# Optimization experiments

Measured on AMD Instinct MI355X. Metric: run time of the kernel, lower is better.

## Reference

```python
import jax, jax.numpy as jnp
import numpy as np

A = 15           # anchors per location (5 sizes x 3 ratios)
H, W = 200, 320  # feature map size
N = 8            # batch
STRIDE = 4
PRE_NMS = 2000
POST_NMS = 1000
NMS_THRESH = 0.7
MIN_SIZE = 1.0
SCORE_THRESH = 0.0
BBOX_CLIP = float(np.log(1000.0 / 16.0))  # torchvision BoxCoder clamp on dw/dh


def _make_anchors():
    # torchvision-style cell anchors: ratio-major, then sizes, shifted over the grid.
    sizes = np.array([32.0, 64.0, 128.0, 256.0, 512.0])
    ratios = np.array([0.5, 1.0, 2.0])
    h_r = np.sqrt(ratios)
    w_r = 1.0 / h_r
    ws = (w_r[:, None] * sizes[None, :]).reshape(-1)  # [15]
    hs = (h_r[:, None] * sizes[None, :]).reshape(-1)
    base = np.stack([-ws, -hs, ws, hs], axis=1) / 2.0  # [15,4] centered at 0
    sx = np.arange(W) * STRIDE
    sy = np.arange(H) * STRIDE
    yy, xx = np.meshgrid(sy, sx, indexing="ij")
    shifts = np.stack([xx, yy, xx, yy], axis=-1).reshape(-1, 1, 4)  # [H*W,1,4]
    return (shifts + base[None]).reshape(-1, 4).astype(np.float32)  # [H*W*A,4]


def setup_inputs() -> dict:
    key = jax.random.key(0)
    k1, k2 = jax.random.split(key)
    return {
        "box_cls": jax.random.normal(k1, (N, A, H, W), dtype=jnp.float32),
        "box_regression": jax.random.normal(k2, (N, 4 * A, H, W), dtype=jnp.float32),
        "anchors": jnp.asarray(_make_anchors()),
        "img_h": 800,
        "img_w": 1280,
    }


def _decode(deltas, anchors):
    # BoxCoder.decode with weights (1,1,1,1). deltas [N,K,4], anchors [K,4] xyxy.
    wa = anchors[:, 2] - anchors[:, 0]
    ha = anchors[:, 3] - anchors[:, 1]
    cxa = anchors[:, 0] + 0.5 * wa
    cya = anchors[:, 1] + 0.5 * ha
    dx, dy = deltas[..., 0], deltas[..., 1]
    dw = jnp.minimum(deltas[..., 2], BBOX_CLIP)
    dh = jnp.minimum(deltas[..., 3], BBOX_CLIP)
    cx = dx * wa + cxa
    cy = dy * ha + cya
    w = wa * jnp.exp(dw)
    h = ha * jnp.exp(dh)
    return jnp.stack(
        [cx - 0.5 * w, cy - 0.5 * h, cx + 0.5 * w, cy + 0.5 * h], axis=-1
    )


def _nms_keep(boxes, scores):
    # Greedy NMS over boxes sorted by descending score; scores < 0 mark invalid.
    x1, y1, x2, y2 = boxes[:, 0], boxes[:, 1], boxes[:, 2], boxes[:, 3]
    area = (x2 - x1) * (y2 - y1)
    ix = jnp.maximum(0.0, jnp.minimum(x2[:, None], x2[None, :]) - jnp.maximum(x1[:, None], x1[None, :]))
    iy = jnp.maximum(0.0, jnp.minimum(y2[:, None], y2[None, :]) - jnp.maximum(y1[:, None], y1[None, :]))
    inter = ix * iy
    iou = inter / (area[:, None] + area[None, :] - inter)  # [K,K]
    k = boxes.shape[0]
    idx = jnp.arange(k)
    keep0 = scores >= 0.0

    def body(i, keep):
        sup = keep[i] & (iou[i] > NMS_THRESH) & (idx > i)
        return keep & ~sup

    return jax.lax.fori_loop(0, k, body, keep0)


def reference(box_cls, box_regression, anchors, img_h, img_w):
    n = box_cls.shape[0]
    # permute_and_flatten: [N, A*C, H, W] -> [N, H*W*A, C]
    objectness = box_cls.reshape(n, A, 1, H, W).transpose(0, 3, 4, 1, 2).reshape(n, -1)
    deltas = box_regression.reshape(n, A, 4, H, W).transpose(0, 3, 4, 1, 2).reshape(n, -1, 4)
    proposals = _decode(deltas, anchors)  # [N, K, 4]
    # clip to image (single image size for the whole batch)
    fh = jnp.float32(img_h)
    fw = jnp.float32(img_w)
    proposals = jnp.stack(
        [
            jnp.clip(proposals[..., 0], 0.0, fw),
            jnp.clip(proposals[..., 1], 0.0, fh),
            jnp.clip(proposals[..., 2], 0.0, fw),
            jnp.clip(proposals[..., 3], 0.0, fh),
        ],
        axis=-1,
    )
    # pre-NMS top-k per image (single feature level)
    top_s, top_i = jax.lax.top_k(objectness, PRE_NMS)        # [N, PRE]
    boxes = jnp.take_along_axis(proposals, top_i[..., None], axis=1)  # [N, PRE, 4]
    scores = jax.nn.sigmoid(top_s)
    # remove small boxes and low-scoring boxes (mask instead of dynamic shapes)
    ws = boxes[..., 2] - boxes[..., 0]
    hs = boxes[..., 3] - boxes[..., 1]
    valid = (ws >= MIN_SIZE) & (hs >= MIN_SIZE) & (scores >= SCORE_THRESH)
    scores_m = jnp.where(valid, scores, -1.0)
    order = jnp.argsort(-scores_m, axis=1)
    boxes_s = jnp.take_along_axis(boxes, order[..., None], axis=1)
    scores_s = jnp.take_along_axis(scores_m, order, axis=1)
    keep = jax.vmap(_nms_keep)(boxes_s, scores_s)            # [N, PRE] bool
    ks = jnp.where(keep, scores_s, -1.0)
    fs, fi = jax.lax.top_k(ks, POST_NMS)                     # [N, POST]
    fb = jnp.take_along_axis(boxes_s, fi[..., None], axis=1)
    ok = fs >= 0.0
    final_boxes = jnp.where(ok[..., None], fb, 0.0)          # zero-padded, fixed shape
    final_scores = jnp.where(ok, fs, 0.0)
    return final_boxes, final_scores
```

## Files before the change

### kernel.cpp

```cpp
#include <hip/hip_runtime.h>
#include <hip/hip_bf16.h>
#include <stdint.h>

typedef unsigned long long u64;

#define AN 15
#define HH 200
#define WW 320
#define HWSZ (HH*WW)
#define PER (AN*HWSZ)
#define NB 8
#define K_PRE 2000
#define K_POST 1000
#define SORTN 4096
#define HBINS 4096
#define HBLK 64
#define FSLICE 512
#define NMS_TH 0.7f
#define BBOX_CLIP_F 4.135166556742356f
#define FLOOR12 3072u

#define PHI(x) ((x) + ((x) >> 3))

__device__ __forceinline__ unsigned keyOfU(unsigned u) {
    return (u & 0x80000000u) ? ~u : (u | 0x80000000u);
}
__device__ __forceinline__ float valOf(unsigned k) {
    unsigned u = (k & 0x80000000u) ? (k ^ 0x80000000u) : ~k;
    return __uint_as_float(u);
}

__global__ __launch_bounds__(256)
void k_hc(const uint4* __restrict__ cls4, u64* __restrict__ fbuf,
          unsigned* __restrict__ cnts) {
    int n = blockIdx.y;
    __shared__ unsigned cnt;
    if (threadIdx.x == 0) cnt = 0;
    __syncthreads();
    u64* slice = fbuf + ((size_t)n * HBLK + blockIdx.x) * FSLICE;
    const uint4* p = cls4 + (size_t)n * (PER / 4);
    int stride = gridDim.x * 256;

#define PROC(vv, ii) {                                                        \
        unsigned kk[4] = {keyOfU((vv).x), keyOfU((vv).y), keyOfU((vv).z),     \
                          keyOfU((vv).w)};                                    \
        int i0 = (ii) * 4;                                                    \
        int a = i0 / HWSZ;                                                    \
        int r0 = i0 - a * HWSZ;                                               \
        _Pragma("unroll")                                                     \
        for (int c = 0; c < 4; ++c) {                                         \
            if ((kk[c] >> 20) >= FLOOR12) {                                   \
                unsigned pos = atomicAdd(&cnt, 1u);                           \
                if (pos < FSLICE) {                                           \
                    unsigned idx = (unsigned)((r0 + c) * AN + a);             \
                    slice[pos] = ((u64)kk[c] << 32) | (u64)(~idx);            \
                }                                                             \
            }                                                                 \
        }                                                                     \
    }

    int i = blockIdx.x * 256 + threadIdx.x;
    for (; i + stride < PER / 4; i += 2 * stride) {
        uint4 a4 = p[i];
        uint4 b4 = p[i + stride];
        PROC(a4, i) PROC(b4, i + stride)
    }
    if (i < PER / 4) { uint4 a4 = p[i]; PROC(a4, i) }
#undef PROC

    __syncthreads();
    unsigned c0 = cnt;
    if (threadIdx.x == 0) cnts[n * HBLK + blockIdx.x] = c0;
    unsigned cz = (c0 > FSLICE) ? FSLICE : c0;
    for (unsigned t = cz + threadIdx.x; t < FSLICE; t += 256) slice[t] = 0ull;
}

__global__ __launch_bounds__(512)
void k_mid(const uint4* __restrict__ cls4, const u64* __restrict__ fbuf,
           const unsigned* __restrict__ cnts, const float* __restrict__ reg,
           const float* __restrict__ anchors, const int* __restrict__ pih,
           const int* __restrict__ piw,
           float* __restrict__ boxes_s, float* __restrict__ scores_s) {
    int n = blockIdx.x;
    int tid = threadIdx.x;
    __shared__ unsigned lh[HBINS];
    __shared__ unsigned L[512];
    __shared__ u64 sb[PHI(SORTN - 1) + 1];
    __shared__ unsigned sT12, sMode, fcnt;

    if (tid < HBLK) L[tid] = cnts[n * HBLK + tid];
    __syncthreads();
    if (tid == 0) {
        unsigned tot = 0; unsigned ovf = 0;
        for (int b = 0; b < HBLK; ++b) { tot += L[b]; ovf |= (L[b] > FSLICE); }
        sMode = (tot >= K_PRE && !ovf) ? 0u : 1u;
    }
    __syncthreads();
    unsigned mode = sMode;

    for (int b = tid; b < HBINS; b += 512) lh[b] = 0;
    __syncthreads();
    if (mode == 0) {
        const u64* src = fbuf + (size_t)n * HBLK * FSLICE;
        for (int t = tid; t < HBLK * FSLICE; t += 512) {
            unsigned k12 = (unsigned)(src[t] >> 52);
            if (k12 >= FLOOR12) atomicAdd(&lh[k12], 1u);
        }
    } else {
        const uint4* p = cls4 + (size_t)n * (PER / 4);
        for (int i = tid; i < PER / 4; i += 512) {
            uint4 v = p[i];
            atomicAdd(&lh[keyOfU(v.x) >> 20], 1u);
            atomicAdd(&lh[keyOfU(v.y) >> 20], 1u);
            atomicAdd(&lh[keyOfU(v.z) >> 20], 1u);
            atomicAdd(&lh[keyOfU(v.w) >> 20], 1u);
        }
    }
    __syncthreads();

    unsigned s[8];
    {
        uint4 v0 = *(const uint4*)(lh + 8 * tid);
        uint4 v1 = *(const uint4*)(lh + 8 * tid + 4);
        s[7] = v1.w; s[6] = v1.z + s[7]; s[5] = v1.y + s[6]; s[4] = v1.x + s[5];
        s[3] = v0.w + s[4]; s[2] = v0.z + s[3]; s[1] = v0.y + s[2]; s[0] = v0.x + s[1];
    }
    __syncthreads();
    L[tid] = s[0];
    __syncthreads();
    for (int off = 1; off < 512; off <<= 1) {
        unsigned x = L[tid] + ((tid + off < 512) ? L[tid + off] : 0u);
        __syncthreads(); L[tid] = x; __syncthreads();
    }
    unsigned tail = (tid < 511) ? L[tid + 1] : 0u;
#pragma unroll
    for (int e = 0; e < 8; ++e) {
        unsigned sfE = s[e] + tail;
        unsigned sfN = (e < 7) ? (s[e + 1] + tail) : tail;
        if (sfE >= K_PRE && sfN < K_PRE) sT12 = 8u * tid + e;
    }
    __syncthreads();
    unsigned T12 = sT12;

    if (tid == 0) fcnt = 0;
    __syncthreads();
    if (mode == 0) {
        const u64* src = fbuf + (size_t)n * HBLK * FSLICE;
        for (int t = tid; t < HBLK * FSLICE; t += 512) {
            u64 e = src[t];
            if ((unsigned)(e >> 52) >= T12) {
                unsigned pos = atomicAdd(&fcnt, 1u);
                if (pos < SORTN) sb[PHI((int)pos)] = e;
            }
        }
    } else {
        const uint4* p = cls4 + (size_t)n * (PER / 4);
        for (int i = tid; i < PER / 4; i += 512) {
            uint4 v = p[i];
            unsigned kk[4] = {keyOfU(v.x), keyOfU(v.y), keyOfU(v.z), keyOfU(v.w)};
            int i0 = i * 4;
            int a = i0 / HWSZ;
            int r0 = i0 - a * HWSZ;
#pragma unroll
            for (int c = 0; c < 4; ++c) {
                if ((kk[c] >> 20) >= T12) {
                    unsigned pos = atomicAdd(&fcnt, 1u);
                    if (pos < SORTN) {
                        unsigned idx = (unsigned)((r0 + c) * AN + a);
                        sb[PHI((int)pos)] = ((u64)kk[c] << 32) | (u64)(~idx);
                    }
                }
            }
        }
    }
    __syncthreads();
    unsigned fc = fcnt; if (fc > SORTN) fc = SORTN;
    for (unsigned t = fc + tid; t < SORTN; t += 512) sb[PHI((int)t)] = 0ull;
    __syncthreads();

    u64 r[8];
#define CE(a_, b_, d_) { bool sw_ = (d_) ? (r[a_] < r[b_]) : (r[a_] > r[b_]); \
                         if (sw_) { u64 t_ = r[a_]; r[a_] = r[b_]; r[b_] = t_; } }
    {
#pragma unroll
        for (int e = 0; e < 8; ++e) r[e] = sb[9 * tid + e];
        CE(0, 1, true)  CE(2, 3, false) CE(4, 5, true)  CE(6, 7, false)
        CE(0, 2, true)  CE(1, 3, true)  CE(4, 6, false) CE(5, 7, false)
        CE(0, 1, true)  CE(2, 3, true)  CE(4, 5, false) CE(6, 7, false)
#pragma unroll
        for (int e = 0; e < 8; ++e) sb[9 * tid + e] = r[e];
        __syncthreads();
    }
    for (int k = 8; k <= SORTN; k <<= 1) {
        for (int j = k >> 1; j >= 8; j >>= 1) {
#pragma unroll
            for (int ss = 0; ss < 4; ++ss) {
                int c = tid + ss * 512;
                int i = ((c & ~(j - 1)) << 1) | (c & (j - 1));
                int p = i | j;
                bool dir = (i & k) == 0;
                u64 a = sb[PHI(i)], b = sb[PHI(p)];
                bool sw = dir ? (a < b) : (a > b);
                if (sw) { sb[PHI(i)] = b; sb[PHI(p)] = a; }
            }
            __syncthreads();
        }
        {
            bool d = ((8 * tid) & k) == 0;
#pragma unroll
            for (int e = 0; e < 8; ++e) r[e] = sb[9 * tid + e];
            CE(0, 4, d) CE(1, 5, d) CE(2, 6, d) CE(3, 7, d)
            CE(0, 2, d) CE(1, 3, d) CE(4, 6, d) CE(5, 7, d)
            CE(0, 1, d) CE(2, 3, d) CE(4, 5, d) CE(6, 7, d)
#pragma unroll
            for (int e = 0; e < 8; ++e) sb[9 * tid + e] = r[e];
            __syncthreads();
        }
    }
#undef CE

    float fh = (float)(*pih);
    float fw = (float)(*piw);

    float bx[4][4]; float sc[4]; int pred[4];
#pragma unroll
    for (int q = 0; q < 4; ++q) {
        int t = tid + 512 * q;
        pred[q] = 0; sc[q] = -1.0f;
        bx[q][0] = bx[q][1] = bx[q][2] = bx[q][3] = 0.f;
        if (t < K_PRE) {
            u64 e = sb[PHI(t)];
            unsigned key = (unsigned)(e >> 32);
            unsigned idx = ~((unsigned)e);
            float v = valOf(key);
            float sgm = 1.0f / (1.0f + expf(-v));
            int a = (int)(idx % AN);
            int rr = (int)(idx / AN);
            size_t base = ((size_t)(n * AN + a) * 4) * HWSZ + rr;
            float dx = reg[base];
            float dy = reg[base + HWSZ];
            float dw = reg[base + 2 * (size_t)HWSZ];
            float dh = reg[base + 3 * (size_t)HWSZ];
            float4 an4 = ((const float4*)anchors)[idx];
            float wa = an4.z - an4.x, ha = an4.w - an4.y;
            float cxa = an4.x + 0.5f * wa, cya = an4.y + 0.5f * ha;
            dw = fminf(dw, BBOX_CLIP_F); dh = fminf(dh, BBOX_CLIP_F);
            float cx = dx * wa + cxa, cy = dy * ha + cya;
            float w = wa * expf(dw), h = ha * expf(dh);
            float x1 = cx - 0.5f * w, y1 = cy - 0.5f * h;
            float x2 = cx + 0.5f * w, y2 = cy + 0.5f * h;
            x1 = fminf(fmaxf(x1, 0.f), fw);
            y1 = fminf(fmaxf(y1, 0.f), fh);
            x2 = fminf(fmaxf(x2, 0.f), fw);
            y2 = fminf(fmaxf(y2, 0.f), fh);
            bool valid = ((x2 - x1) >= 1.0f) && ((y2 - y1) >= 1.0f);
            bx[q][0] = x1; bx[q][1] = y1; bx[q][2] = x2; bx[q][3] = y2;
            sc[q] = sgm; pred[q] = valid ? 1 : 0;
        }
    }
    __syncthreads();

    __shared__ u64 ww[32];
    __shared__ int wpfx[33];
    int lane = tid & 63, wid = tid >> 6;
#pragma unroll
    for (int q = 0; q < 4; ++q) {
        u64 bal = __ballot(pred[q] != 0);
        if (lane == 0) ww[wid + 8 * q] = bal;
    }
    __syncthreads();
    if (tid == 0) {
        int acc = 0;
#pragma unroll
        for (int w2 = 0; w2 < 32; ++w2) { wpfx[w2] = acc; acc += (int)__popcll(ww[w2]); }
        wpfx[32] = acc;
    }
    __syncthreads();
    int V = wpfx[32];

#pragma unroll
    for (int q = 0; q < 4; ++q) {
        int t = tid + 512 * q;
        if (t < K_PRE) {
            int wi = t >> 6;
            int before = wpfx[wi] + (int)__popcll(ww[wi] & ((1ull << (unsigned)lane) - 1ull));
            int pos = pred[q] ? before : (V + (t - before));
            float4 b4; b4.x = bx[q][0]; b4.y = bx[q][1]; b4.z = bx[q][2]; b4.w = bx[q][3];
            ((float4*)boxes_s)[(size_t)n * K_PRE + pos] = b4;
            scores_s[(size_t)n * K_PRE + pos] = pred[q] ? sc[q] : -1.0f;
        }
    }
}

__global__ __launch_bounds__(64)
void k_maskT(const float* __restrict__ boxes_s, u64* __restrict__ maskT) {
    int n = blockIdx.y;
    int p = blockIdx.x;
    int lane = threadIdx.x;
    int cb = (int)((sqrtf(8.0f * (float)p + 1.0f) - 1.0f) * 0.5f);
    while ((cb + 1) * (cb + 2) / 2 <= p) ++cb;
    while (cb * (cb + 1) / 2 > p) --cb;
    int rb = p - cb * (cb + 1) / 2;

    __shared__ float rx1[64], ry1[64], rx2[64], ry2[64], rar[64];
    int c = cb * 64 + lane;
    bool cok = c < K_PRE;
    float4 c4; c4.x = c4.y = c4.z = c4.w = 0.f;
    if (cok) c4 = ((const float4*)boxes_s)[(size_t)n * K_PRE + c];
    float areaC = (c4.z - c4.x) * (c4.w - c4.y);

    int r = rb * 64 + lane;
    float4 r4; r4.x = r4.y = r4.z = r4.w = 0.f;
    if (r < K_PRE) r4 = ((const float4*)boxes_s)[(size_t)n * K_PRE + r];
    rx1[lane] = r4.x; ry1[lane] = r4.y; rx2[lane] = r4.z; ry2[lane] = r4.w;
    rar[lane] = (r4.z - r4.x) * (r4.w - r4.y);
    __syncthreads();

    u64 bits = 0;
    int bmax = 0;
    if (cok) { bmax = c - rb * 64; if (bmax > 64) bmax = 64; }
    for (int b = 0; b < bmax; ++b) {
        float ix = fminf(c4.z, rx2[b]) - fmaxf(c4.x, rx1[b]); ix = fmaxf(ix, 0.f);
        float iy = fminf(c4.w, ry2[b]) - fmaxf(c4.y, ry1[b]); iy = fmaxf(iy, 0.f);
        float inter = ix * iy;
        float iou = inter / (rar[b] + areaC - inter);
        if (iou > NMS_TH) bits |= (1ull << b);
    }
    maskT[((size_t)n * 32 + rb) * 2048 + c] = bits;
}

__global__ __launch_bounds__(64)
void k_scanT(const u64* __restrict__ maskT, const float* __restrict__ boxes_s,
             const float* __restrict__ scores_s, float* __restrict__ out) {
    int n = blockIdx.x;
    int lane = threadIdx.x;
    __shared__ float ls[2048];
    __shared__ u64 keptw[32];
    for (int i = lane; i < 500; i += 64)
        ((float4*)ls)[i] = ((const float4*)(scores_s + (size_t)n * K_PRE))[i];
    if (lane < 48) ls[2000 + lane] = -1.0f;
    if (lane < 32) keptw[lane] = 0ull;
    __syncthreads();

    const u64* mb = maskT + (size_t)n * 32 * 2048;
    int kept_total = 0;

    u64 wv[32];
#pragma unroll
    for (int rb = 0; rb < 32; ++rb) wv[rb] = mb[(size_t)rb * 2048 + lane];

    for (int f = 0; f < 32; ++f) {
        int c = f * 64 + lane;

        u64 wn[32];
        if (f < 31) {
            int cn = c + 64;
#pragma unroll
            for (int rb = 0; rb < 32; ++rb) wn[rb] = mb[(size_t)rb * 2048 + cn];
        }

        u64 hit = 0;
#pragma unroll
        for (int rb = 0; rb < 32; ++rb) hit |= (wv[rb] & keptw[rb]);
        bool ext = hit != 0ull;
        u64 diag = wv[f];

        bool v = (ls[c] >= 0.0f) && !ext;
        u64 kept = __ballot(v);
        while (true) {
            u64 nk = __ballot(v && ((diag & kept) == 0ull));
            if (nk == kept) break;
            kept = nk;
        }

        if ((kept >> lane) & 1ull) {
            int rank = kept_total + (int)__popcll(kept & ((1ull << lane) - 1ull));
            if (rank < K_POST) {
                float4 b4 = ((const float4*)boxes_s)[(size_t)n * K_PRE + c];
                ((float4*)out)[(size_t)n * K_POST + rank] = b4;
                out[(size_t)NB * K_POST * 4 + (size_t)n * K_POST + rank] = ls[c];
            }
        }
        kept_total += (int)__popcll(kept);
        if (lane == 0) keptw[f] = kept;
        if (kept_total >= K_POST || f == 31) break;
#pragma unroll
        for (int rb = 0; rb < 32; ++rb) wv[rb] = wn[rb];
    }

    int start = (kept_total < K_POST) ? kept_total : K_POST;
    float4 z4; z4.x = z4.y = z4.z = z4.w = 0.f;
    for (int rk = start + lane; rk < K_POST; rk += 64) {
        ((float4*)out)[(size_t)n * K_POST + rk] = z4;
        out[(size_t)NB * K_POST * 4 + (size_t)n * K_POST + rk] = 0.f;
    }
}

extern "C" void kernel_launch(void* const* d_in, const int* in_sizes, int n_in,
                              void* d_out, int out_size, void* d_ws, size_t ws_size,
                              hipStream_t stream) {
    const float* cls     = (const float*)d_in[0];
    const float* regr    = (const float*)d_in[1];
    const float* anchors = (const float*)d_in[2];
    const int*   pih     = (const int*)d_in[3];
    const int*   piw     = (const int*)d_in[4];
    float* out = (float*)d_out;

    char* w = (char*)d_ws;
    u64*      maskT   = (u64*)(w + 0);
    u64*      fbuf    = (u64*)(w + 4194304);
    unsigned* cnts    = (unsigned*)(w + 6291456);
    float*    boxes_s = (float*)(w + 6293504);
    float*    scores_s= (float*)(w + 6549504);

    k_hc<<<dim3(HBLK, NB), 256, 0, stream>>>((const uint4*)cls, fbuf, cnts);
    k_mid<<<NB, 512, 0, stream>>>((const uint4*)cls, fbuf, cnts, regr, anchors,
                                  pih, piw, boxes_s, scores_s);
    k_maskT<<<dim3(528, NB), 64, 0, stream>>>(boxes_s, maskT);
    k_scanT<<<NB, 64, 0, stream>>>(maskT, boxes_s, scores_s, out);
    (void)in_sizes; (void)n_in; (void)ws_size; (void)out_size;
}
```

Baseline: 144.1 us.

## Split k_mid into separate select, sort and decode kernels

The monolithic per-image k_mid kernel becomes three kernels. k_select builds the histogram and finds the threshold with 1024 threads. k_sort gathers candidates and bitonic-sorts them in shared memory, then writes the top entries to a global candidate buffer. k_decode decodes boxes and compacts valid ones with 1024 threads. The aim is to give each phase a leaner kernel with less shared memory and register pressure and more threads where the work is parallel. In exchange it adds two kernel launches and a global round-trip for the sorted candidates, and still runs only one block per image.

```diff
diff --git a/kernel.cpp b/kernel.cpp
--- a/kernel.cpp
+++ b/kernel.cpp
@@ -75,40 +75,35 @@
     for (unsigned t = cz + threadIdx.x; t < FSLICE; t += 256) slice[t] = 0ull;
 }
 
-__global__ __launch_bounds__(512)
-void k_mid(const uint4* __restrict__ cls4, const u64* __restrict__ fbuf,
-           const unsigned* __restrict__ cnts, const float* __restrict__ reg,
-           const float* __restrict__ anchors, const int* __restrict__ pih,
-           const int* __restrict__ piw,
-           float* __restrict__ boxes_s, float* __restrict__ scores_s) {
-    int n = blockIdx.x;
-    int tid = threadIdx.x;
+__global__ __launch_bounds__(1024)
+void k_select(const uint4* __restrict__ cls4, const u64* __restrict__ fbuf,
+              const unsigned* __restrict__ cnts,
+              unsigned* __restrict__ selT12, unsigned* __restrict__ modeArr) {
+    int n = blockIdx.x, t = threadIdx.x;
     __shared__ unsigned lh[HBINS];
-    __shared__ unsigned L[512];
-    __shared__ u64 sb[PHI(SORTN - 1) + 1];
-    __shared__ unsigned sT12, sMode, fcnt;
-
-    if (tid < HBLK) L[tid] = cnts[n * HBLK + tid];
-    __syncthreads();
-    if (tid == 0) {
-        unsigned tot = 0; unsigned ovf = 0;
+    __shared__ unsigned L[1024];
+    __shared__ unsigned sMode;
+
+    if (t < HBLK) L[t] = cnts[n * HBLK + t];
+    for (int b = t; b < HBINS; b += 1024) lh[b] = 0;
+    __syncthreads();
+    if (t == 0) {
+        unsigned tot = 0, ovf = 0;
         for (int b = 0; b < HBLK; ++b) { tot += L[b]; ovf |= (L[b] > FSLICE); }
         sMode = (tot >= K_PRE && !ovf) ? 0u : 1u;
     }
     __syncthreads();
     unsigned mode = sMode;
 
-    for (int b = tid; b < HBINS; b += 512) lh[b] = 0;
-    __syncthreads();
     if (mode == 0) {
         const u64* src = fbuf + (size_t)n * HBLK * FSLICE;
-        for (int t = tid; t < HBLK * FSLICE; t += 512) {
-            unsigned k12 = (unsigned)(src[t] >> 52);
+        for (int s = t; s < HBLK * FSLICE; s += 1024) {
+            unsigned k12 = (unsigned)(src[s] >> 52);
             if (k12 >= FLOOR12) atomicAdd(&lh[k12], 1u);
         }
     } else {
         const uint4* p = cls4 + (size_t)n * (PER / 4);
-        for (int i = tid; i < PER / 4; i += 512) {
+        for (int i = t; i < PER / 4; i += 1024) {
             uint4 v = p[i];
             atomicAdd(&lh[keyOfU(v.x) >> 20], 1u);
             atomicAdd(&lh[keyOfU(v.y) >> 20], 1u);
@@ -118,38 +113,43 @@
     }
     __syncthreads();
 
-    unsigned s[8];
-    {
-        uint4 v0 = *(const uint4*)(lh + 8 * tid);
-        uint4 v1 = *(const uint4*)(lh + 8 * tid + 4);
-        s[7] = v1.w; s[6] = v1.z + s[7]; s[5] = v1.y + s[6]; s[4] = v1.x + s[5];
-        s[3] = v0.w + s[4]; s[2] = v0.z + s[3]; s[1] = v0.y + s[2]; s[0] = v0.x + s[1];
-    }
-    __syncthreads();
-    L[tid] = s[0];
-    __syncthreads();
-    for (int off = 1; off < 512; off <<= 1) {
-        unsigned x = L[tid] + ((tid + off < 512) ? L[tid + off] : 0u);
-        __syncthreads(); L[tid] = x; __syncthreads();
-    }
-    unsigned tail = (tid < 511) ? L[tid + 1] : 0u;
-#pragma unroll
-    for (int e = 0; e < 8; ++e) {
-        unsigned sfE = s[e] + tail;
-        unsigned sfN = (e < 7) ? (s[e + 1] + tail) : tail;
-        if (sfE >= K_PRE && sfN < K_PRE) sT12 = 8u * tid + e;
-    }
-    __syncthreads();
-    unsigned T12 = sT12;
-
-    if (tid == 0) fcnt = 0;
-    __syncthreads();
+    uint4 v = *(const uint4*)(lh + 4 * t);
+    unsigned sf[5];
+    sf[3] = v.w; sf[2] = v.z + sf[3]; sf[1] = v.y + sf[2]; sf[0] = v.x + sf[1];
+    __syncthreads();
+    L[t] = sf[0];
+    __syncthreads();
+    for (int off = 1; off < 1024; off <<= 1) {
+        unsigned x = L[t] + ((t + off < 1024) ? L[t + off] : 0u);
+        __syncthreads(); L[t] = x; __syncthreads();
+    }
+    unsigned tail = (t < 1023) ? L[t + 1] : 0u;
+    sf[0] += tail; sf[1] += tail; sf[2] += tail; sf[3] += tail; sf[4] = tail;
+#pragma unroll
+    for (int e = 0; e < 4; ++e)
+        if (sf[e] >= K_PRE && sf[e + 1] < K_PRE) selT12[n] = 4u * t + e;
+    if (t == 0) modeArr[n] = mode;
+}
+
+__global__ __launch_bounds__(512)
+void k_sort(const uint4* __restrict__ cls4, const u64* __restrict__ fbuf,
+            const unsigned* __restrict__ selT12, const unsigned* __restrict__ modeArr,
+            u64* __restrict__ cand) {
+    int n = blockIdx.x;
+    int tid = threadIdx.x;
+    __shared__ u64 sb[PHI(SORTN - 1) + 1];
+    __shared__ unsigned cnt;
+    if (tid == 0) cnt = 0;
+    __syncthreads();
+    unsigned T12 = selT12[n];
+    unsigned mode = modeArr[n];
+
     if (mode == 0) {
         const u64* src = fbuf + (size_t)n * HBLK * FSLICE;
-        for (int t = tid; t < HBLK * FSLICE; t += 512) {
-            u64 e = src[t];
+        for (int s = tid; s < HBLK * FSLICE; s += 512) {
+            u64 e = src[s];
             if ((unsigned)(e >> 52) >= T12) {
-                unsigned pos = atomicAdd(&fcnt, 1u);
+                unsigned pos = atomicAdd(&cnt, 1u);
                 if (pos < SORTN) sb[PHI((int)pos)] = e;
             }
         }
@@ -164,7 +164,7 @@
 #pragma unroll
             for (int c = 0; c < 4; ++c) {
                 if ((kk[c] >> 20) >= T12) {
-                    unsigned pos = atomicAdd(&fcnt, 1u);
+                    unsigned pos = atomicAdd(&cnt, 1u);
                     if (pos < SORTN) {
                         unsigned idx = (unsigned)((r0 + c) * AN + a);
                         sb[PHI((int)pos)] = ((u64)kk[c] << 32) | (u64)(~idx);
@@ -174,13 +174,14 @@
         }
     }
     __syncthreads();
-    unsigned fc = fcnt; if (fc > SORTN) fc = SORTN;
-    for (unsigned t = fc + tid; t < SORTN; t += 512) sb[PHI((int)t)] = 0ull;
+    unsigned c0 = cnt; if (c0 > SORTN) c0 = SORTN;
+    for (unsigned t = c0 + tid; t < SORTN; t += 512) sb[PHI((int)t)] = 0ull;
     __syncthreads();
 
     u64 r[8];
 #define CE(a_, b_, d_) { bool sw_ = (d_) ? (r[a_] < r[b_]) : (r[a_] > r[b_]); \
                          if (sw_) { u64 t_ = r[a_]; r[a_] = r[b_]; r[b_] = t_; } }
+
     {
 #pragma unroll
         for (int e = 0; e < 8; ++e) r[e] = sb[9 * tid + e];
@@ -191,11 +192,12 @@
         for (int e = 0; e < 8; ++e) sb[9 * tid + e] = r[e];
         __syncthreads();
     }
+
     for (int k = 8; k <= SORTN; k <<= 1) {
         for (int j = k >> 1; j >= 8; j >>= 1) {
 #pragma unroll
-            for (int ss = 0; ss < 4; ++ss) {
-                int c = tid + ss * 512;
+            for (int s = 0; s < 4; ++s) {
+                int c = tid + s * 512;
                 int i = ((c & ~(j - 1)) << 1) | (c & (j - 1));
                 int p = i | j;
                 bool dir = (i & k) == 0;
@@ -219,21 +221,32 @@
     }
 #undef CE
 
+    for (int t = tid; t < K_PRE; t += 512)
+        cand[(size_t)n * SORTN + t] = sb[PHI(t)];
+}
+
+__global__ __launch_bounds__(1024)
+void k_decode(const float* __restrict__ reg, const float* __restrict__ anchors,
+              const int* __restrict__ pih, const int* __restrict__ piw,
+              const u64* __restrict__ cand,
+              float* __restrict__ boxes_s, float* __restrict__ scores_s) {
+    int n = blockIdx.x;
+    int tid = threadIdx.x;
     float fh = (float)(*pih);
     float fw = (float)(*piw);
 
-    float bx[4][4]; float sc[4]; int pred[4];
-#pragma unroll
-    for (int q = 0; q < 4; ++q) {
-        int t = tid + 512 * q;
+    float bx[2][4]; float sc[2]; int pred[2];
+#pragma unroll
+    for (int q = 0; q < 2; ++q) {
+        int t = tid + 1024 * q;
         pred[q] = 0; sc[q] = -1.0f;
         bx[q][0] = bx[q][1] = bx[q][2] = bx[q][3] = 0.f;
         if (t < K_PRE) {
-            u64 e = sb[PHI(t)];
+            u64 e = cand[(size_t)n * SORTN + t];
             unsigned key = (unsigned)(e >> 32);
             unsigned idx = ~((unsigned)e);
             float v = valOf(key);
-            float sgm = 1.0f / (1.0f + expf(-v));
+            float s = 1.0f / (1.0f + expf(-v));
             int a = (int)(idx % AN);
             int rr = (int)(idx / AN);
             size_t base = ((size_t)(n * AN + a) * 4) * HWSZ + rr;
@@ -255,32 +268,31 @@
             y2 = fminf(fmaxf(y2, 0.f), fh);
             bool valid = ((x2 - x1) >= 1.0f) && ((y2 - y1) >= 1.0f);
             bx[q][0] = x1; bx[q][1] = y1; bx[q][2] = x2; bx[q][3] = y2;
-            sc[q] = sgm; pred[q] = valid ? 1 : 0;
-        }
-    }
-    __syncthreads();
+            sc[q] = s; pred[q] = valid ? 1 : 0;
+        }
+    }
 
     __shared__ u64 ww[32];
     __shared__ int wpfx[33];
     int lane = tid & 63, wid = tid >> 6;
 #pragma unroll
-    for (int q = 0; q < 4; ++q) {
+    for (int q = 0; q < 2; ++q) {
         u64 bal = __ballot(pred[q] != 0);
-        if (lane == 0) ww[wid + 8 * q] = bal;
+        if (lane == 0) ww[wid + 16 * q] = bal;
     }
     __syncthreads();
     if (tid == 0) {
-        int acc = 0;
-#pragma unroll
-        for (int w2 = 0; w2 < 32; ++w2) { wpfx[w2] = acc; acc += (int)__popcll(ww[w2]); }
-        wpfx[32] = acc;
+        int s = 0;
+#pragma unroll
+        for (int w2 = 0; w2 < 32; ++w2) { wpfx[w2] = s; s += (int)__popcll(ww[w2]); }
+        wpfx[32] = s;
     }
     __syncthreads();
     int V = wpfx[32];
 
 #pragma unroll
-    for (int q = 0; q < 4; ++q) {
-        int t = tid + 512 * q;
+    for (int q = 0; q < 2; ++q) {
+        int t = tid + 1024 * q;
         if (t < K_PRE) {
             int wi = t >> 6;
             int before = wpfx[wi] + (int)__popcll(ww[wi] & ((1ull << (unsigned)lane) - 1ull));
@@ -410,12 +422,17 @@
     u64*      maskT   = (u64*)(w + 0);
     u64*      fbuf    = (u64*)(w + 4194304);
     unsigned* cnts    = (unsigned*)(w + 6291456);
-    float*    boxes_s = (float*)(w + 6293504);
-    float*    scores_s= (float*)(w + 6549504);
+    unsigned* selT12  = (unsigned*)(w + 6293504);
+    unsigned* modeArr = (unsigned*)(w + 6293568);
+    u64*      cand    = (u64*)(w + 6293632);
+    float*    boxes_s = (float*)(w + 6555776);
+    float*    scores_s= (float*)(w + 6811776);
 
     k_hc<<<dim3(HBLK, NB), 256, 0, stream>>>((const uint4*)cls, fbuf, cnts);
-    k_mid<<<NB, 512, 0, stream>>>((const uint4*)cls, fbuf, cnts, regr, anchors,
-                                  pih, piw, boxes_s, scores_s);
+    k_select<<<NB, 1024, 0, stream>>>((const uint4*)cls, fbuf, cnts, selT12, modeArr);
+    k_sort<<<NB, 512, 0, stream>>>((const uint4*)cls, fbuf, selT12, modeArr, cand);
+    k_decode<<<NB, 1024, 0, stream>>>(regr, anchors, pih, piw,
+                                      cand, boxes_s, scores_s);
     k_maskT<<<dim3(528, NB), 64, 0, stream>>>(boxes_s, maskT);
     k_scanT<<<NB, 64, 0, stream>>>(maskT, boxes_s, scores_s, out);
     (void)in_sizes; (void)n_in; (void)ws_size; (void)out_size;
```

Measured after the change: 137.1 us. 1.05x faster.
